# Performance work log

Measured on AMD Instinct MI355X. Metric: run time of the kernel, lower is better.

## Reference

```python
import jax, jax.numpy as jnp
import numpy as np

D_MODEL = 512
WINDOW = 8
N_LAYERS = 3
BATCH = 16384
EPS = 1e-12  # torch F.normalize eps


def _l2norm(x):
    # normalize over last axis, matching torch.nn.functional.normalize(p=2)
    n = jnp.sqrt(jnp.sum(x * x, axis=-1, keepdims=True))
    return x / jnp.maximum(n, EPS)


def setup_inputs() -> dict:
    key = jax.random.key(0)
    ks = jax.random.split(key, 14)
    d, w, L = D_MODEL, WINDOW, N_LAYERS
    s = 1.0 / np.sqrt(d)
    inp = {
        "x": jax.random.normal(ks[0], (BATCH, w + 1, d), dtype=jnp.float32),
        # stacked per-layer params
        "Wq": jax.random.normal(ks[1], (L, d, d), dtype=jnp.float32) * s,
        "bq": jax.random.normal(ks[2], (L, d), dtype=jnp.float32) * s,
        "Wk": jax.random.normal(ks[3], (L, w + 1, d, d), dtype=jnp.float32) * s,  # grouped conv: per-position linear
        "bk": jax.random.normal(ks[4], (L, w + 1, d), dtype=jnp.float32) * s,
        "Wfw": jax.random.normal(ks[5], (L, w, d, d), dtype=jnp.float32) * s,
        "bfw": jax.random.normal(ks[6], (L, w, d), dtype=jnp.float32) * s,
        "Wfc": jax.random.normal(ks[7], (L, d, d), dtype=jnp.float32) * s,
        "bfc": jax.random.normal(ks[8], (L, d), dtype=jnp.float32) * s,
        # final layer params
        "Wqf": jax.random.normal(ks[9], (d, d), dtype=jnp.float32) * s,
        "bqf": jax.random.normal(ks[10], (d,), dtype=jnp.float32) * s,
        "Wkf": jax.random.normal(ks[11], (w + 1, d, d), dtype=jnp.float32) * s,
        "bkf": jax.random.normal(ks[12], (w + 1, d), dtype=jnp.float32) * s,
    }
    return inp


def _attn_cent(x, Wq, bq, Wk, bk):
    # q: Linear on last position; k: grouped conv == per-position linear
    xc = x[:, -1, :]                                   # [B, d]
    q = xc @ Wq.T + bq                                 # [B, d]
    k = jnp.einsum('bpe,pde->bpd', x, Wk) + bk         # [B, W+1, d]
    attns = jax.nn.softmax(jnp.einsum('bd,bpd->bp', q, k), axis=-1)
    x_cent = jnp.einsum('bp,bpd->bd', attns, x)        # [B, d]
    return xc, x_cent


def _pt_layer(x, Wq, bq, Wk, bk, Wfw, bfw, Wfc, bfc):
    xc, x_cent = _attn_cent(x, Wq, bq, Wk, bk)
    x_cent = _l2norm(x_cent)
    x_cent = x_cent @ Wfc.T + bfc                      # ff_cent (dropout = identity, eval)
    x_cent = _l2norm(x_cent + xc)
    xw = x[:, :-1, :]                                  # [B, W, d]
    x_window = jnp.einsum('bpe,pde->bpd', xw, Wfw) + bfw + xw
    x_window = _l2norm(x_window)
    return jnp.concatenate([x_window, x_cent[:, None, :]], axis=1)


def reference(x, Wq, bq, Wk, bk, Wfw, bfw, Wfc, bfc, Wqf, bqf, Wkf, bkf):
    for l in range(N_LAYERS):
        x = _pt_layer(x, Wq[l], bq[l], Wk[l], bk[l], Wfw[l], bfw[l], Wfc[l], bfc[l])
    # final layer
    xc, x_cent = _attn_cent(x, Wqf, bqf, Wkf, bkf)
    return _l2norm((x_cent + xc)[:, None, :])          # [B, 1, d]
```

## Files before the change

### kernel.cpp

```cpp
#include <hip/hip_runtime.h>

#define BATCH_N 16384
#define PLANE 262144
typedef unsigned short ushort_t;
typedef __attribute__((ext_vector_type(4))) float f32x4;
typedef __attribute__((ext_vector_type(8))) short s16x8;
typedef __attribute__((ext_vector_type(4))) unsigned short u16x4;

__device__ inline void split_bf(float f, ushort_t& h, ushort_t& l) {
    unsigned u = __float_as_uint(f);
    h = (ushort_t)(u >> 16);
    float fh = __uint_as_float(u & 0xFFFF0000u);
    float r = f - fh;
    l = (ushort_t)(__float_as_uint(r) >> 16);
}

__global__ __launch_bounds__(256) void convert_w_k(
    const float* __restrict__ src, ushort_t* __restrict__ hi,
    ushort_t* __restrict__ lo, int n4)
{
    const int i = blockIdx.x * 256 + threadIdx.x;
    if (i >= n4) return;
    const f32x4 v = ((const f32x4*)src)[i];
    ushort_t h[4], l[4];
#pragma unroll
    for (int u = 0; u < 4; ++u) split_bf(v[u], h[u], l[u]);
    *(u16x4*)&hi[(size_t)i * 4] = (u16x4){h[0], h[1], h[2], h[3]};
    *(u16x4*)&lo[(size_t)i * 4] = (u16x4){l[0], l[1], l[2], l[3]};
}

template <int EPI>
__global__ __launch_bounds__(256, 3) void mfma_gemm_k(
    const float* __restrict__ A, int lda, int aoff,
    const ushort_t* __restrict__ Wh, const ushort_t* __restrict__ Wl,
    const float* __restrict__ bias, float* __restrict__ outp,
    const float* __restrict__ q, float* __restrict__ logits)
{
    __shared__ __align__(16) ushort_t Ah[128 * 40];
    __shared__ __align__(16) ushort_t Al[128 * 40];
    __shared__ __align__(16) ushort_t Bh[128 * 40];
    __shared__ __align__(16) ushort_t Bl[128 * 40];

    const int t = threadIdx.x;
    const int lane = t & 63, wave = t >> 6;
    const int wm = (wave >> 1) * 64, wn = (wave & 1) * 64;
    const int quad = lane >> 4, l15 = lane & 15;
    const size_t b0 = (size_t)blockIdx.x * 128;
    const int n0 = blockIdx.y * 128;
    int p = 0;
    if (EPI == 1) {
        p = blockIdx.z;
        Wh += (size_t)PLANE * p;
        Wl += (size_t)PLANE * p;
        aoff += p * 512;
    }

    f32x4 acc[4][4] = {};

    for (int k0 = 0; k0 < 512; k0 += 32) {
        f32x4 av[4];
        s16x8 bhv[2], blv[2];
#pragma unroll
        for (int u = 0; u < 4; ++u) {
            const int f = t + 256 * u, row = f >> 3, c = f & 7;
            av[u] = *(const f32x4*)&A[(b0 + row) * lda + aoff + k0 + c * 4];
        }
#pragma unroll
        for (int u = 0; u < 2; ++u) {
            const int f = t + 256 * u, row = f >> 2, c = f & 3;
            bhv[u] = *(const s16x8*)&Wh[(size_t)(n0 + row) * 512 + k0 + c * 8];
            blv[u] = *(const s16x8*)&Wl[(size_t)(n0 + row) * 512 + k0 + c * 8];
        }
        __syncthreads();
#pragma unroll
        for (int u = 0; u < 4; ++u) {
            const int f = t + 256 * u, row = f >> 3, c = f & 7;
            ushort_t h[4], l[4];
#pragma unroll
            for (int e = 0; e < 4; ++e) split_bf(av[u][e], h[e], l[e]);
            *(u16x4*)&Ah[row * 40 + c * 4] = (u16x4){h[0], h[1], h[2], h[3]};
            *(u16x4*)&Al[row * 40 + c * 4] = (u16x4){l[0], l[1], l[2], l[3]};
        }
#pragma unroll
        for (int u = 0; u < 2; ++u) {
            const int f = t + 256 * u, row = f >> 2, c = f & 3;
            *(s16x8*)&Bh[row * 40 + c * 8] = bhv[u];
            *(s16x8*)&Bl[row * 40 + c * 8] = blv[u];
        }
        __syncthreads();
        s16x8 ah[4], alo[4];
#pragma unroll
        for (int i = 0; i < 4; ++i) {
            ah[i]  = *(const s16x8*)&Ah[(wm + i * 16 + l15) * 40 + quad * 8];
            alo[i] = *(const s16x8*)&Al[(wm + i * 16 + l15) * 40 + quad * 8];
        }
#pragma unroll
        for (int j = 0; j < 4; ++j) {
            const s16x8 bh = *(const s16x8*)&Bh[(wn + j * 16 + l15) * 40 + quad * 8];
            const s16x8 bl = *(const s16x8*)&Bl[(wn + j * 16 + l15) * 40 + quad * 8];
#pragma unroll
            for (int i = 0; i < 4; ++i) {
                acc[i][j] = __builtin_amdgcn_mfma_f32_16x16x32_bf16(ah[i], bh, acc[i][j], 0, 0, 0);
                acc[i][j] = __builtin_amdgcn_mfma_f32_16x16x32_bf16(ah[i], bl, acc[i][j], 0, 0, 0);
                acc[i][j] = __builtin_amdgcn_mfma_f32_16x16x32_bf16(alo[i], bh, acc[i][j], 0, 0, 0);
            }
        }
    }

    if (EPI == 0) {
#pragma unroll
        for (int i = 0; i < 4; ++i) {
            const int gm0 = (int)b0 + wm + i * 16 + quad * 4;
#pragma unroll
            for (int j = 0; j < 4; ++j) {
                const int gn = n0 + wn + j * 16 + l15;
                const float bv = bias[gn];
#pragma unroll
                for (int r = 0; r < 4; ++r)
                    outp[(size_t)(gm0 + r) * 512 + gn] = acc[i][j][r] + bv;
            }
        }
    } else {
        float rp[4][4] = {};
#pragma unroll
        for (int i = 0; i < 4; ++i) {
            const int gm0 = (int)b0 + wm + i * 16 + quad * 4;
#pragma unroll
            for (int j = 0; j < 4; ++j) {
                const int gn = n0 + wn + j * 16 + l15;
                const float bv = bias[(size_t)p * 512 + gn];
#pragma unroll
                for (int r = 0; r < 4; ++r)
                    rp[i][r] += (acc[i][j][r] + bv) * q[(size_t)(gm0 + r) * 512 + gn];
            }
        }
#pragma unroll
        for (int m = 1; m < 16; m <<= 1)
#pragma unroll
            for (int i = 0; i < 4; ++i)
#pragma unroll
                for (int r = 0; r < 4; ++r)
                    rp[i][r] += __shfl_xor(rp[i][r], m, 64);
        if (l15 == 0) {
#pragma unroll
            for (int i = 0; i < 4; ++i) {
                const int gm0 = (int)b0 + wm + i * 16 + quad * 4;
#pragma unroll
                for (int r = 0; r < 4; ++r)
                    atomicAdd(&logits[(size_t)(gm0 + r) * 9 + p], rp[i][r]);
            }
        }
    }
}

__global__ __launch_bounds__(256) void softmax_cent_k(
    const float* __restrict__ x, const float* __restrict__ logits,
    float* __restrict__ outp, int mode)
{
    const int lane = threadIdx.x & 63;
    const size_t b = (size_t)blockIdx.x * 4 + (threadIdx.x >> 6);
    float lg[9], m = -1e30f;
#pragma unroll
    for (int p = 0; p < 9; ++p) { lg[p] = logits[b * 9 + p]; m = fmaxf(m, lg[p]); }
    float s = 0.f;
#pragma unroll
    for (int p = 0; p < 9; ++p) { lg[p] = __expf(lg[p] - m); s += lg[p]; }
    const float inv = 1.0f / s;
    f32x4 c[2];
    float ssq = 0.f;
#pragma unroll
    for (int v = 0; v < 2; ++v) {
        f32x4 a = {0.f, 0.f, 0.f, 0.f};
#pragma unroll
        for (int p = 0; p < 9; ++p) {
            const f32x4 xv = ((const f32x4*)&x[(b * 9 + p) * 512])[v * 64 + lane];
            a += lg[p] * xv;
        }
        a *= inv;
        if (mode) a += ((const f32x4*)&x[(b * 9 + 8) * 512])[v * 64 + lane];
        c[v] = a;
        ssq += a[0]*a[0] + a[1]*a[1] + a[2]*a[2] + a[3]*a[3];
    }
#pragma unroll
    for (int off = 32; off > 0; off >>= 1) ssq += __shfl_xor(ssq, off, 64);
    const float invn = 1.0f / fmaxf(sqrtf(ssq), 1e-12f);
#pragma unroll
    for (int v = 0; v < 2; ++v)
        ((f32x4*)&outp[b * 512])[v * 64 + lane] = c[v] * invn;
}

__global__ __launch_bounds__(256) void resid_norm_k(
    float* __restrict__ dst, int dstride, const float* __restrict__ src)
{
    const int lane = threadIdx.x & 63;
    const size_t b = (size_t)blockIdx.x * 4 + (threadIdx.x >> 6);
    f32x4* d4 = (f32x4*)&dst[b * (size_t)dstride];
    const f32x4* s4 = (const f32x4*)&src[b * 512];
    f32x4 a[2];
    float ssq = 0.f;
#pragma unroll
    for (int v = 0; v < 2; ++v) {
        a[v] = d4[v * 64 + lane] + s4[v * 64 + lane];
        ssq += a[v][0]*a[v][0] + a[v][1]*a[v][1] + a[v][2]*a[v][2] + a[v][3]*a[v][3];
    }
#pragma unroll
    for (int off = 32; off > 0; off >>= 1) ssq += __shfl_xor(ssq, off, 64);
    const float invn = 1.0f / fmaxf(sqrtf(ssq), 1e-12f);
#pragma unroll
    for (int v = 0; v < 2; ++v) d4[v * 64 + lane] = a[v] * invn;
}

extern "C" void kernel_launch(void* const* d_in, const int* in_sizes, int n_in,
                              void* d_out, int out_size, void* d_ws, size_t ws_size,
                              hipStream_t stream) {
    (void)in_sizes; (void)n_in; (void)out_size; (void)ws_size;
    float* x = (float*)d_in[0];
    const float* Wq  = (const float*)d_in[1];
    const float* bq  = (const float*)d_in[2];
    const float* Wk  = (const float*)d_in[3];
    const float* bk  = (const float*)d_in[4];
    const float* Wfw = (const float*)d_in[5];
    const float* bfw = (const float*)d_in[6];
    const float* Wfc = (const float*)d_in[7];
    const float* bfc = (const float*)d_in[8];
    const float* Wqf = (const float*)d_in[9];
    const float* bqf = (const float*)d_in[10];
    const float* Wkf = (const float*)d_in[11];
    const float* bkf = (const float*)d_in[12];
    float* out = (float*)d_out;

    ushort_t* whi = (ushort_t*)d_ws;
    ushort_t* wlo = whi + (size_t)67 * PLANE;
    float* fbuf   = (float*)(wlo + (size_t)67 * PLANE);
    float* q      = fbuf;
    float* cent   = q    + (size_t)BATCH_N * 512;
    float* y      = cent + (size_t)BATCH_N * 512;
    float* logits = y    + (size_t)BATCH_N * 512;
    float* tmp    = cent;

    const size_t OWq = 0, OWk = 3, OWfw = 30, OWfc = 54, OWqf = 57, OWkf = 58;

    struct { const float* s; size_t off; int cnt; } cv[6] = {
        {Wq, OWq, 3}, {Wk, OWk, 27}, {Wfw, OWfw, 24},
        {Wfc, OWfc, 3}, {Wqf, OWqf, 1}, {Wkf, OWkf, 9}};
    for (int i = 0; i < 6; ++i) {
        const int n4 = cv[i].cnt * PLANE / 4;
        convert_w_k<<<(n4 + 255) / 256, 256, 0, stream>>>(
            cv[i].s, whi + cv[i].off * PLANE, wlo + cv[i].off * PLANE, n4);
    }

    const dim3 gemm_grid(BATCH_N / 128, 4);
    const dim3 log_grid(BATCH_N / 128, 4, 9);
    const int ew_grid = BATCH_N / 4;

    for (int l = 0; l < 3; ++l) {
        mfma_gemm_k<0><<<gemm_grid, 256, 0, stream>>>(
            x, 9 * 512, 8 * 512,
            whi + (OWq + l) * PLANE, wlo + (OWq + l) * PLANE,
            bq + l * 512, q, nullptr, nullptr);
        hipMemsetAsync(logits, 0, (size_t)BATCH_N * 9 * sizeof(float), stream);
        mfma_gemm_k<1><<<log_grid, 256, 0, stream>>>(
            x, 9 * 512, 0,
            whi + (OWk + (size_t)l * 9) * PLANE, wlo + (OWk + (size_t)l * 9) * PLANE,
            bk + (size_t)l * 9 * 512, nullptr, q, logits);
        softmax_cent_k<<<ew_grid, 256, 0, stream>>>(x, logits, cent, 0);
        mfma_gemm_k<0><<<gemm_grid, 256, 0, stream>>>(
            cent, 512, 0,
            whi + (OWfc + l) * PLANE, wlo + (OWfc + l) * PLANE,
            bfc + l * 512, y, nullptr, nullptr);
        resid_norm_k<<<ew_grid, 256, 0, stream>>>(x + 8 * 512, 9 * 512, y);
        for (int p = 0; p < 8; ++p) {
            mfma_gemm_k<0><<<gemm_grid, 256, 0, stream>>>(
                x, 9 * 512, p * 512,
                whi + (OWfw + (size_t)l * 8 + p) * PLANE,
                wlo + (OWfw + (size_t)l * 8 + p) * PLANE,
                bfw + ((size_t)l * 8 + p) * 512, tmp, nullptr, nullptr);
            resid_norm_k<<<ew_grid, 256, 0, stream>>>(x + p * 512, 9 * 512, tmp);
        }
    }
    mfma_gemm_k<0><<<gemm_grid, 256, 0, stream>>>(
        x, 9 * 512, 8 * 512, whi + OWqf * PLANE, wlo + OWqf * PLANE,
        bqf, q, nullptr, nullptr);
    hipMemsetAsync(logits, 0, (size_t)BATCH_N * 9 * sizeof(float), stream);
    mfma_gemm_k<1><<<log_grid, 256, 0, stream>>>(
        x, 9 * 512, 0, whi + OWkf * PLANE, wlo + OWkf * PLANE,
        bkf, nullptr, q, logits);
    softmax_cent_k<<<ew_grid, 256, 0, stream>>>(x, logits, out, 1);
}
```

Before: 3.075 ms.

## Rewrite GEMM pipeline with fused residual-norm epilogues and packed split-bf16 activations

Replaces the 128x128 GEMM with a 64-row by full-512-column tile kernel that uses direct global-to-LDS loads for pre-swizzled weight planes. The residual add and L2 normalize are fused into the GEMM epilogue, which removes the separate resid_norm kernels and the temp buffers. The 8 per-position window GEMMs and the 9 key GEMMs now run as one grid each using the z dimension. Logits are reduced inside each block, so the atomics and the memset go away. Activations after layer 0 are stored in place as packed hi/lo bf16 words, which cuts conversion work but changes the in-memory format of x and relies on the in-place writes being race-free.

After: 3.336 ms. 8.5% more time.

```diff
diff --git a/kernel.cpp b/kernel.cpp
--- a/kernel.cpp
+++ b/kernel.cpp
@@ -1,213 +1,330 @@
 #include <hip/hip_runtime.h>
 
 #define BATCH_N 16384
+#define LDA 4608
 #define PLANE 262144
 typedef unsigned short ushort_t;
 typedef __attribute__((ext_vector_type(4))) float f32x4;
 typedef __attribute__((ext_vector_type(8))) short s16x8;
-typedef __attribute__((ext_vector_type(4))) unsigned short u16x4;
-
-__device__ inline void split_bf(float f, ushort_t& h, ushort_t& l) {
+typedef __attribute__((ext_vector_type(4))) unsigned u32x4;
+
+__device__ __forceinline__ void split_bf(float f, ushort_t& h, ushort_t& l) {
     unsigned u = __float_as_uint(f);
     h = (ushort_t)(u >> 16);
-    float fh = __uint_as_float(u & 0xFFFF0000u);
-    float r = f - fh;
+    float r = f - __uint_as_float(u & 0xFFFF0000u);
     l = (ushort_t)(__float_as_uint(r) >> 16);
+}
+__device__ __forceinline__ unsigned pack_bf(float f) {
+    unsigned u = __float_as_uint(f);
+    float r = f - __uint_as_float(u & 0xFFFF0000u);
+    return (u & 0xFFFF0000u) | (__float_as_uint(r) >> 16);
+}
+__device__ __forceinline__ float upack(unsigned u) {
+    return __uint_as_float(u & 0xFFFF0000u) + __uint_as_float(u << 16);
+}
+__device__ __forceinline__ s16x8 mk8(const ushort_t* v) {
+    return (s16x8){(short)v[0],(short)v[1],(short)v[2],(short)v[3],
+                   (short)v[4],(short)v[5],(short)v[6],(short)v[7]};
+}
+typedef __attribute__((address_space(3))) unsigned as3_u32;
+typedef __attribute__((address_space(1))) unsigned as1_u32;
+__device__ __forceinline__ void dma16(const ushort_t* g, ushort_t* l) {
+    __builtin_amdgcn_global_load_lds((as1_u32*)(unsigned long long)g,
+                                     (as3_u32*)(unsigned)(unsigned long long)l,
+                                     16, 0, 0);
 }
 
 __global__ __launch_bounds__(256) void convert_w_k(
     const float* __restrict__ src, ushort_t* __restrict__ hi,
-    ushort_t* __restrict__ lo, int n4)
+    ushort_t* __restrict__ lo, int total)
 {
-    const int i = blockIdx.x * 256 + threadIdx.x;
-    if (i >= n4) return;
-    const f32x4 v = ((const f32x4*)src)[i];
-    ushort_t h[4], l[4];
-#pragma unroll
-    for (int u = 0; u < 4; ++u) split_bf(v[u], h[u], l[u]);
-    *(u16x4*)&hi[(size_t)i * 4] = (u16x4){h[0], h[1], h[2], h[3]};
-    *(u16x4*)&lo[(size_t)i * 4] = (u16x4){l[0], l[1], l[2], l[3]};
-}
-
-template <int EPI>
-__global__ __launch_bounds__(256, 3) void mfma_gemm_k(
-    const float* __restrict__ A, int lda, int aoff,
-    const ushort_t* __restrict__ Wh, const ushort_t* __restrict__ Wl,
-    const float* __restrict__ bias, float* __restrict__ outp,
-    const float* __restrict__ q, float* __restrict__ logits)
+    const int gid = blockIdx.x * 256 + threadIdx.x;
+    if (gid >= total) return;
+    const int pp = gid >> 15;
+    const int rem = gid & 32767;
+    const int n = rem >> 6;
+    const int o = rem & 63;
+    const int chunk = o >> 2, oct = o & 3;
+    const float* s = src + (size_t)pp * PLANE + (size_t)n * 512 + o * 8;
+    const f32x4 f0 = *(const f32x4*)s;
+    const f32x4 f1 = *(const f32x4*)(s + 4);
+    ushort_t h[8], l[8];
+#pragma unroll
+    for (int e = 0; e < 4; ++e) {
+        split_bf(f0[e], h[e], l[e]);
+        split_bf(f1[e], h[4 + e], l[4 + e]);
+    }
+    const size_t d = (size_t)pp * PLANE + ((size_t)chunk * 512 + n) * 32
+                   + (size_t)((oct ^ (n & 3)) * 8);
+    *(s16x8*)&hi[d] = mk8(h);
+    *(s16x8*)&lo[d] = mk8(l);
+}
+
+template<int EPI, int AFMT, int RFMT>
+__global__ __launch_bounds__(256, 2) void gemm64_k(
+    const void* Ap, int lda, int aoff0, int a_zstep,
+    const ushort_t* __restrict__ Wh0, const ushort_t* __restrict__ Wl0,
+    const float* __restrict__ bias0,
+    float* __restrict__ outp,
+    const float* __restrict__ qv, float* __restrict__ logits,
+    void* resid, int rstride, int roff0)
 {
-    __shared__ __align__(16) ushort_t Ah[128 * 40];
-    __shared__ __align__(16) ushort_t Al[128 * 40];
-    __shared__ __align__(16) ushort_t Bh[128 * 40];
-    __shared__ __align__(16) ushort_t Bl[128 * 40];
+    __shared__ ushort_t smem[20480];
+    ushort_t* Bh = smem;
+    ushort_t* Bl = smem + 8192;
+    ushort_t* Ah = smem + 16384;
+    ushort_t* Al = smem + 18432;
 
     const int t = threadIdx.x;
-    const int lane = t & 63, wave = t >> 6;
-    const int wm = (wave >> 1) * 64, wn = (wave & 1) * 64;
+    const int lane = t & 63;
+    const int w = t >> 6;
     const int quad = lane >> 4, l15 = lane & 15;
-    const size_t b0 = (size_t)blockIdx.x * 128;
-    const int n0 = blockIdx.y * 128;
-    int p = 0;
-    if (EPI == 1) {
-        p = blockIdx.z;
-        Wh += (size_t)PLANE * p;
-        Wl += (size_t)PLANE * p;
-        aoff += p * 512;
-    }
-
-    f32x4 acc[4][4] = {};
-
-    for (int k0 = 0; k0 < 512; k0 += 32) {
-        f32x4 av[4];
-        s16x8 bhv[2], blv[2];
-#pragma unroll
-        for (int u = 0; u < 4; ++u) {
-            const int f = t + 256 * u, row = f >> 3, c = f & 7;
-            av[u] = *(const f32x4*)&A[(b0 + row) * lda + aoff + k0 + c * 4];
-        }
-#pragma unroll
-        for (int u = 0; u < 2; ++u) {
-            const int f = t + 256 * u, row = f >> 2, c = f & 3;
-            bhv[u] = *(const s16x8*)&Wh[(size_t)(n0 + row) * 512 + k0 + c * 8];
-            blv[u] = *(const s16x8*)&Wl[(size_t)(n0 + row) * 512 + k0 + c * 8];
+    const int b0 = blockIdx.x * 64;
+    const int pz = blockIdx.z;
+    const int aoff = aoff0 + pz * a_zstep;
+    const ushort_t* Wh = Wh0 + (size_t)pz * PLANE;
+    const ushort_t* Wl = Wl0 + (size_t)pz * PLANE;
+    const float* bias = bias0 + pz * 512;
+
+    const int arow = t >> 2;
+    const int aoct = t & 3;
+    const size_t abase = (size_t)(b0 + arow) * lda + aoff + aoct * 8;
+    const int adst = arow * 32 + ((aoct ^ (arow & 3)) * 8);
+
+    f32x4 acc[4][8] = {};
+
+    for (int c = 0; c < 16; ++c) {
+        ushort_t h8[8], l8[8];
+        if (AFMT == 1) {
+            const unsigned* Au = (const unsigned*)Ap;
+            const u32x4 u0 = *(const u32x4*)(Au + abase + (size_t)c * 32);
+            const u32x4 u1 = *(const u32x4*)(Au + abase + (size_t)c * 32 + 4);
+#pragma unroll
+            for (int e = 0; e < 4; ++e) {
+                h8[e] = (ushort_t)(u0[e] >> 16); l8[e] = (ushort_t)u0[e];
+                h8[4+e] = (ushort_t)(u1[e] >> 16); l8[4+e] = (ushort_t)u1[e];
+            }
+        } else {
+            const float* Af = (const float*)Ap;
+            const f32x4 f0 = *(const f32x4*)(Af + abase + (size_t)c * 32);
+            const f32x4 f1 = *(const f32x4*)(Af + abase + (size_t)c * 32 + 4);
+#pragma unroll
+            for (int e = 0; e < 4; ++e) {
+                split_bf(f0[e], h8[e], l8[e]);
+                split_bf(f1[e], h8[4+e], l8[4+e]);
+            }
+        }
+        s16x8 ah[4], av[4];
+#pragma unroll
+        for (int h = 0; h < 2; ++h) {
+            __syncthreads();
+            {
+                const size_t srow = ((size_t)c * 512 + h * 256 + w * 64) * 32
+                                  + (size_t)lane * 8;
+#pragma unroll
+                for (int u = 0; u < 4; ++u) {
+                    dma16(Wh + srow + u * 512, Bh + (w * 4 + u) * 512);
+                    dma16(Wl + srow + u * 512, Bl + (w * 4 + u) * 512);
+                }
+            }
+            if (h == 0) {
+                *(s16x8*)&Ah[adst] = mk8(h8);
+                *(s16x8*)&Al[adst] = mk8(l8);
+            }
+            __syncthreads();
+            if (h == 0) {
+#pragma unroll
+                for (int i = 0; i < 4; ++i) {
+                    const int rr = i * 16 + l15;
+                    const int ao = rr * 32 + ((quad ^ (rr & 3)) * 8);
+                    ah[i] = *(const s16x8*)&Ah[ao];
+                    av[i] = *(const s16x8*)&Al[ao];
+                }
+            }
+#pragma unroll
+            for (int j2 = 0; j2 < 4; ++j2) {
+                const int rn = w * 64 + j2 * 16 + l15;
+                const int bo = rn * 32 + ((quad ^ (rn & 3)) * 8);
+                const s16x8 bh = *(const s16x8*)&Bh[bo];
+                const s16x8 bl = *(const s16x8*)&Bl[bo];
+#pragma unroll
+                for (int i = 0; i < 4; ++i) {
+                    f32x4 a = acc[i][h * 4 + j2];
+                    a = __builtin_amdgcn_mfma_f32_16x16x32_bf16(av[i], bh, a, 0, 0, 0);
+                    a = __builtin_amdgcn_mfma_f32_16x16x32_bf16(ah[i], bl, a, 0, 0, 0);
+                    a = __builtin_amdgcn_mfma_f32_16x16x32_bf16(ah[i], bh, a, 0, 0, 0);
+                    acc[i][h * 4 + j2] = a;
+                }
+            }
+        }
+    }
+
+    __syncthreads();
+    float* red = (float*)smem;
+    float* nrm = (float*)smem + 256;
+
+    if (EPI == 0) {
+#pragma unroll
+        for (int i = 0; i < 4; ++i)
+#pragma unroll
+        for (int j = 0; j < 8; ++j) {
+            const int n = (j >> 2) * 256 + w * 64 + (j & 3) * 16 + l15;
+            const float bv = bias[n];
+#pragma unroll
+            for (int r = 0; r < 4; ++r) {
+                const int m = i * 16 + quad * 4 + r;
+                outp[(size_t)(b0 + m) * 512 + n] = acc[i][j][r] + bv;
+            }
+        }
+    } else if (EPI == 1) {
+        float rp[16];
+#pragma unroll
+        for (int v = 0; v < 16; ++v) rp[v] = 0.f;
+#pragma unroll
+        for (int j = 0; j < 8; ++j) {
+            const int n = (j >> 2) * 256 + w * 64 + (j & 3) * 16 + l15;
+            const float bv = bias[n];
+#pragma unroll
+            for (int i = 0; i < 4; ++i)
+#pragma unroll
+            for (int r = 0; r < 4; ++r) {
+                const int m = i * 16 + quad * 4 + r;
+                rp[i * 4 + r] += (acc[i][j][r] + bv) * qv[(size_t)(b0 + m) * 512 + n];
+            }
+        }
+#pragma unroll
+        for (int msk = 1; msk < 16; msk <<= 1)
+#pragma unroll
+            for (int v = 0; v < 16; ++v) rp[v] += __shfl_xor(rp[v], msk, 64);
+        if (l15 == 0) {
+#pragma unroll
+            for (int i = 0; i < 4; ++i)
+#pragma unroll
+            for (int r = 0; r < 4; ++r)
+                red[(i * 16 + quad * 4 + r) * 4 + w] = rp[i * 4 + r];
         }
         __syncthreads();
-#pragma unroll
-        for (int u = 0; u < 4; ++u) {
-            const int f = t + 256 * u, row = f >> 3, c = f & 7;
-            ushort_t h[4], l[4];
-#pragma unroll
-            for (int e = 0; e < 4; ++e) split_bf(av[u][e], h[e], l[e]);
-            *(u16x4*)&Ah[row * 40 + c * 4] = (u16x4){h[0], h[1], h[2], h[3]};
-            *(u16x4*)&Al[row * 40 + c * 4] = (u16x4){l[0], l[1], l[2], l[3]};
-        }
-#pragma unroll
-        for (int u = 0; u < 2; ++u) {
-            const int f = t + 256 * u, row = f >> 2, c = f & 3;
-            *(s16x8*)&Bh[row * 40 + c * 8] = bhv[u];
-            *(s16x8*)&Bl[row * 40 + c * 8] = blv[u];
+        if (t < 64)
+            logits[(size_t)(b0 + t) * 9 + pz] =
+                red[t * 4] + red[t * 4 + 1] + red[t * 4 + 2] + red[t * 4 + 3];
+    } else {
+        const int roffE = roff0 + pz * a_zstep;
+        float rp[16];
+#pragma unroll
+        for (int v = 0; v < 16; ++v) rp[v] = 0.f;
+#pragma unroll
+        for (int j = 0; j < 8; ++j) {
+            const int n = (j >> 2) * 256 + w * 64 + (j & 3) * 16 + l15;
+            const float bv = bias[n];
+#pragma unroll
+            for (int i = 0; i < 4; ++i)
+#pragma unroll
+            for (int r = 0; r < 4; ++r) {
+                const int m = i * 16 + quad * 4 + r;
+                const size_t ridx = (size_t)(b0 + m) * rstride + roffE + n;
+                const float rv = (RFMT == 1) ? upack(((const unsigned*)resid)[ridx])
+                                             : ((const float*)resid)[ridx];
+                const float v = acc[i][j][r] + bv + rv;
+                acc[i][j][r] = v;
+                rp[i * 4 + r] += v * v;
+            }
+        }
+#pragma unroll
+        for (int msk = 1; msk < 16; msk <<= 1)
+#pragma unroll
+            for (int v = 0; v < 16; ++v) rp[v] += __shfl_xor(rp[v], msk, 64);
+        if (l15 == 0) {
+#pragma unroll
+            for (int i = 0; i < 4; ++i)
+#pragma unroll
+            for (int r = 0; r < 4; ++r)
+                red[(i * 16 + quad * 4 + r) * 4 + w] = rp[i * 4 + r];
         }
         __syncthreads();
-        s16x8 ah[4], alo[4];
-#pragma unroll
-        for (int i = 0; i < 4; ++i) {
-            ah[i]  = *(const s16x8*)&Ah[(wm + i * 16 + l15) * 40 + quad * 8];
-            alo[i] = *(const s16x8*)&Al[(wm + i * 16 + l15) * 40 + quad * 8];
-        }
-#pragma unroll
-        for (int j = 0; j < 4; ++j) {
-            const s16x8 bh = *(const s16x8*)&Bh[(wn + j * 16 + l15) * 40 + quad * 8];
-            const s16x8 bl = *(const s16x8*)&Bl[(wn + j * 16 + l15) * 40 + quad * 8];
-#pragma unroll
-            for (int i = 0; i < 4; ++i) {
-                acc[i][j] = __builtin_amdgcn_mfma_f32_16x16x32_bf16(ah[i], bh, acc[i][j], 0, 0, 0);
-                acc[i][j] = __builtin_amdgcn_mfma_f32_16x16x32_bf16(ah[i], bl, acc[i][j], 0, 0, 0);
-                acc[i][j] = __builtin_amdgcn_mfma_f32_16x16x32_bf16(alo[i], bh, acc[i][j], 0, 0, 0);
-            }
-        }
-    }
-
-    if (EPI == 0) {
-#pragma unroll
-        for (int i = 0; i < 4; ++i) {
-            const int gm0 = (int)b0 + wm + i * 16 + quad * 4;
-#pragma unroll
-            for (int j = 0; j < 4; ++j) {
-                const int gn = n0 + wn + j * 16 + l15;
-                const float bv = bias[gn];
-#pragma unroll
-                for (int r = 0; r < 4; ++r)
-                    outp[(size_t)(gm0 + r) * 512 + gn] = acc[i][j][r] + bv;
-            }
-        }
-    } else {
-        float rp[4][4] = {};
-#pragma unroll
-        for (int i = 0; i < 4; ++i) {
-            const int gm0 = (int)b0 + wm + i * 16 + quad * 4;
-#pragma unroll
-            for (int j = 0; j < 4; ++j) {
-                const int gn = n0 + wn + j * 16 + l15;
-                const float bv = bias[(size_t)p * 512 + gn];
-#pragma unroll
-                for (int r = 0; r < 4; ++r)
-                    rp[i][r] += (acc[i][j][r] + bv) * q[(size_t)(gm0 + r) * 512 + gn];
-            }
-        }
-#pragma unroll
-        for (int m = 1; m < 16; m <<= 1)
-#pragma unroll
-            for (int i = 0; i < 4; ++i)
-#pragma unroll
-                for (int r = 0; r < 4; ++r)
-                    rp[i][r] += __shfl_xor(rp[i][r], m, 64);
-        if (l15 == 0) {
-#pragma unroll
-            for (int i = 0; i < 4; ++i) {
-                const int gm0 = (int)b0 + wm + i * 16 + quad * 4;
-#pragma unroll
-                for (int r = 0; r < 4; ++r)
-                    atomicAdd(&logits[(size_t)(gm0 + r) * 9 + p], rp[i][r]);
-            }
-        }
-    }
-}
-
+        if (t < 64) {
+            const float s = red[t * 4] + red[t * 4 + 1] + red[t * 4 + 2] + red[t * 4 + 3];
+            nrm[t] = 1.0f / fmaxf(sqrtf(s), 1e-12f);
+        }
+        __syncthreads();
+        unsigned* xw = (unsigned*)resid;
+#pragma unroll
+        for (int i = 0; i < 4; ++i)
+#pragma unroll
+        for (int r = 0; r < 4; ++r) {
+            const int m = i * 16 + quad * 4 + r;
+            const float s = nrm[m];
+#pragma unroll
+            for (int j = 0; j < 8; ++j) {
+                const int n = (j >> 2) * 256 + w * 64 + (j & 3) * 16 + l15;
+                xw[(size_t)(b0 + m) * rstride + roffE + n] = pack_bf(acc[i][j][r] * s);
+            }
+        }
+    }
+}
+
+template<int XFMT, int MODE>
 __global__ __launch_bounds__(256) void softmax_cent_k(
-    const float* __restrict__ x, const float* __restrict__ logits,
-    float* __restrict__ outp, int mode)
+    const void* xg, const float* __restrict__ logits, void* outp)
 {
     const int lane = threadIdx.x & 63;
     const size_t b = (size_t)blockIdx.x * 4 + (threadIdx.x >> 6);
-    float lg[9], m = -1e30f;
-#pragma unroll
-    for (int p = 0; p < 9; ++p) { lg[p] = logits[b * 9 + p]; m = fmaxf(m, lg[p]); }
+    float lg[9], mx = -1e30f;
+#pragma unroll
+    for (int p = 0; p < 9; ++p) { lg[p] = logits[b * 9 + p]; mx = fmaxf(mx, lg[p]); }
     float s = 0.f;
 #pragma unroll
-    for (int p = 0; p < 9; ++p) { lg[p] = __expf(lg[p] - m); s += lg[p]; }
+    for (int p = 0; p < 9; ++p) { lg[p] = __expf(lg[p] - mx); s += lg[p]; }
     const float inv = 1.0f / s;
-    f32x4 c[2];
+    float c[8];
     float ssq = 0.f;
 #pragma unroll
     for (int v = 0; v < 2; ++v) {
-        f32x4 a = {0.f, 0.f, 0.f, 0.f};
+        float a[4] = {0.f, 0.f, 0.f, 0.f};
+        float x8[4] = {0.f, 0.f, 0.f, 0.f};
 #pragma unroll
         for (int p = 0; p < 9; ++p) {
-            const f32x4 xv = ((const f32x4*)&x[(b * 9 + p) * 512])[v * 64 + lane];
-            a += lg[p] * xv;
-        }
-        a *= inv;
-        if (mode) a += ((const f32x4*)&x[(b * 9 + 8) * 512])[v * 64 + lane];
-        c[v] = a;
-        ssq += a[0]*a[0] + a[1]*a[1] + a[2]*a[2] + a[3]*a[3];
+            float f[4];
+            if (XFMT == 1) {
+                const u32x4 u = ((const u32x4*)xg)[(size_t)(b * 9 + p) * 128 + v * 64 + lane];
+#pragma unroll
+                for (int e = 0; e < 4; ++e) f[e] = upack(u[e]);
+            } else {
+                const f32x4 xv = ((const f32x4*)xg)[(size_t)(b * 9 + p) * 128 + v * 64 + lane];
+#pragma unroll
+                for (int e = 0; e < 4; ++e) f[e] = xv[e];
+            }
+#pragma unroll
+            for (int e = 0; e < 4; ++e) a[e] += lg[p] * f[e];
+            if (MODE == 1 && p == 8) {
+#pragma unroll
+                for (int e = 0; e < 4; ++e) x8[e] = f[e];
+            }
+        }
+#pragma unroll
+        for (int e = 0; e < 4; ++e) {
+            float av = a[e] * inv;
+            if (MODE == 1) av += x8[e];
+            c[v * 4 + e] = av;
+            ssq += av * av;
+        }
     }
 #pragma unroll
     for (int off = 32; off > 0; off >>= 1) ssq += __shfl_xor(ssq, off, 64);
     const float invn = 1.0f / fmaxf(sqrtf(ssq), 1e-12f);
 #pragma unroll
-    for (int v = 0; v < 2; ++v)
-        ((f32x4*)&outp[b * 512])[v * 64 + lane] = c[v] * invn;
-}
-
-__global__ __launch_bounds__(256) void resid_norm_k(
-    float* __restrict__ dst, int dstride, const float* __restrict__ src)
-{
-    const int lane = threadIdx.x & 63;
-    const size_t b = (size_t)blockIdx.x * 4 + (threadIdx.x >> 6);
-    f32x4* d4 = (f32x4*)&dst[b * (size_t)dstride];
-    const f32x4* s4 = (const f32x4*)&src[b * 512];
-    f32x4 a[2];
-    float ssq = 0.f;
-#pragma unroll
     for (int v = 0; v < 2; ++v) {
-        a[v] = d4[v * 64 + lane] + s4[v * 64 + lane];
-        ssq += a[v][0]*a[v][0] + a[v][1]*a[v][1] + a[v][2]*a[v][2] + a[v][3]*a[v][3];
-    }
-#pragma unroll
-    for (int off = 32; off > 0; off >>= 1) ssq += __shfl_xor(ssq, off, 64);
-    const float invn = 1.0f / fmaxf(sqrtf(ssq), 1e-12f);
-#pragma unroll
-    for (int v = 0; v < 2; ++v) d4[v * 64 + lane] = a[v] * invn;
+        if (MODE == 1) {
+            f32x4 o;
+#pragma unroll
+            for (int e = 0; e < 4; ++e) o[e] = c[v * 4 + e] * invn;
+            ((f32x4*)outp)[(size_t)b * 128 + v * 64 + lane] = o;
+        } else {
+            u32x4 o;
+#pragma unroll
+            for (int e = 0; e < 4; ++e) o[e] = pack_bf(c[v * 4 + e] * invn);
+            ((u32x4*)outp)[(size_t)b * 128 + v * 64 + lane] = o;
+        }
+    }
 }
 
 extern "C" void kernel_launch(void* const* d_in, const int* in_sizes, int n_in,
@@ -231,59 +348,56 @@
 
     ushort_t* whi = (ushort_t*)d_ws;
     ushort_t* wlo = whi + (size_t)67 * PLANE;
-    float* fbuf   = (float*)(wlo + (size_t)67 * PLANE);
-    float* q      = fbuf;
-    float* cent   = q    + (size_t)BATCH_N * 512;
-    float* y      = cent + (size_t)BATCH_N * 512;
-    float* logits = y    + (size_t)BATCH_N * 512;
-    float* tmp    = cent;
+    float* q       = (float*)(wlo + (size_t)67 * PLANE);
+    unsigned* cent = (unsigned*)(q + (size_t)BATCH_N * 512);
+    float* logits  = (float*)(cent + (size_t)BATCH_N * 512);
 
     const size_t OWq = 0, OWk = 3, OWfw = 30, OWfc = 54, OWqf = 57, OWkf = 58;
-
     struct { const float* s; size_t off; int cnt; } cv[6] = {
         {Wq, OWq, 3}, {Wk, OWk, 27}, {Wfw, OWfw, 24},
         {Wfc, OWfc, 3}, {Wqf, OWqf, 1}, {Wkf, OWkf, 9}};
-    for (int i = 0; i < 6; ++i) {
-        const int n4 = cv[i].cnt * PLANE / 4;
-        convert_w_k<<<(n4 + 255) / 256, 256, 0, stream>>>(
-            cv[i].s, whi + cv[i].off * PLANE, wlo + cv[i].off * PLANE, n4);
-    }
-
-    const dim3 gemm_grid(BATCH_N / 128, 4);
-    const dim3 log_grid(BATCH_N / 128, 4, 9);
-    const int ew_grid = BATCH_N / 4;
+    for (int i = 0; i < 6; ++i)
+        convert_w_k<<<cv[i].cnt * 128, 256, 0, stream>>>(
+            cv[i].s, whi + cv[i].off * PLANE, wlo + cv[i].off * PLANE,
+            cv[i].cnt * 32768);
+
+    const dim3 g1(BATCH_N / 64, 1, 1);
+    const dim3 g8(BATCH_N / 64, 1, 8);
+    const dim3 g9(BATCH_N / 64, 1, 9);
+    const int sg = BATCH_N / 4;
 
     for (int l = 0; l < 3; ++l) {
-        mfma_gemm_k<0><<<gemm_grid, 256, 0, stream>>>(
-            x, 9 * 512, 8 * 512,
-            whi + (OWq + l) * PLANE, wlo + (OWq + l) * PLANE,
-            bq + l * 512, q, nullptr, nullptr);
-        hipMemsetAsync(logits, 0, (size_t)BATCH_N * 9 * sizeof(float), stream);
-        mfma_gemm_k<1><<<log_grid, 256, 0, stream>>>(
-            x, 9 * 512, 0,
-            whi + (OWk + (size_t)l * 9) * PLANE, wlo + (OWk + (size_t)l * 9) * PLANE,
-            bk + (size_t)l * 9 * 512, nullptr, q, logits);
-        softmax_cent_k<<<ew_grid, 256, 0, stream>>>(x, logits, cent, 0);
-        mfma_gemm_k<0><<<gemm_grid, 256, 0, stream>>>(
-            cent, 512, 0,
-            whi + (OWfc + l) * PLANE, wlo + (OWfc + l) * PLANE,
-            bfc + l * 512, y, nullptr, nullptr);
-        resid_norm_k<<<ew_grid, 256, 0, stream>>>(x + 8 * 512, 9 * 512, y);
-        for (int p = 0; p < 8; ++p) {
-            mfma_gemm_k<0><<<gemm_grid, 256, 0, stream>>>(
-                x, 9 * 512, p * 512,
-                whi + (OWfw + (size_t)l * 8 + p) * PLANE,
-                wlo + (OWfw + (size_t)l * 8 + p) * PLANE,
-                bfw + ((size_t)l * 8 + p) * 512, tmp, nullptr, nullptr);
-            resid_norm_k<<<ew_grid, 256, 0, stream>>>(x + p * 512, 9 * 512, tmp);
-        }
-    }
-    mfma_gemm_k<0><<<gemm_grid, 256, 0, stream>>>(
-        x, 9 * 512, 8 * 512, whi + OWqf * PLANE, wlo + OWqf * PLANE,
-        bqf, q, nullptr, nullptr);
-    hipMemsetAsync(logits, 0, (size_t)BATCH_N * 9 * sizeof(float), stream);
-    mfma_gemm_k<1><<<log_grid, 256, 0, stream>>>(
-        x, 9 * 512, 0, whi + OWkf * PLANE, wlo + OWkf * PLANE,
-        bkf, nullptr, q, logits);
-    softmax_cent_k<<<ew_grid, 256, 0, stream>>>(x, logits, out, 1);
-}
+        const ushort_t* qh = whi + (OWq + l) * PLANE,  * ql = wlo + (OWq + l) * PLANE;
+        const ushort_t* kh = whi + (OWk + (size_t)l * 9) * PLANE,
+                      * kl = wlo + (OWk + (size_t)l * 9) * PLANE;
+        const ushort_t* ch = whi + (OWfc + l) * PLANE, * cl = wlo + (OWfc + l) * PLANE;
+        const ushort_t* fh = whi + (OWfw + (size_t)l * 8) * PLANE,
+                      * fl = wlo + (OWfw + (size_t)l * 8) * PLANE;
+        if (l == 0) {
+            gemm64_k<0,0,0><<<g1,256,0,stream>>>(x, LDA, 8*512, 0, qh, ql,
+                bq, q, nullptr, nullptr, nullptr, 0, 0);
+            gemm64_k<1,0,0><<<g9,256,0,stream>>>(x, LDA, 0, 512, kh, kl,
+                bk, nullptr, q, logits, nullptr, 0, 0);
+            softmax_cent_k<0,0><<<sg,256,0,stream>>>(x, logits, cent);
+            gemm64_k<2,1,0><<<g1,256,0,stream>>>(cent, 512, 0, 0, ch, cl,
+                bfc, nullptr, nullptr, nullptr, x, LDA, 8*512);
+            gemm64_k<2,0,0><<<g8,256,0,stream>>>(x, LDA, 0, 512, fh, fl,
+                bfw, nullptr, nullptr, nullptr, x, LDA, 0);
+        } else {
+            gemm64_k<0,1,0><<<g1,256,0,stream>>>(x, LDA, 8*512, 0, qh, ql,
+                bq + l*512, q, nullptr, nullptr, nullptr, 0, 0);
+            gemm64_k<1,1,0><<<g9,256,0,stream>>>(x, LDA, 0, 512, kh, kl,
+                bk + (size_t)l*9*512, nullptr, q, logits, nullptr, 0, 0);
+            softmax_cent_k<1,0><<<sg,256,0,stream>>>(x, logits, cent);
+            gemm64_k<2,1,1><<<g1,256,0,stream>>>(cent, 512, 0, 0, ch, cl,
+                bfc + l*512, nullptr, nullptr, nullptr, x, LDA, 8*512);
+            gemm64_k<2,1,1><<<g8,256,0,stream>>>(x, LDA, 0, 512, fh, fl,
+                bfw + (size_t)l*8*512, nullptr, nullptr, nullptr, x, LDA, 0);
+        }
+    }
+    gemm64_k<0,1,0><<<g1,256,0,stream>>>(x, LDA, 8*512, 0,
+        whi + OWqf*PLANE, wlo + OWqf*PLANE, bqf, q, nullptr, nullptr, nullptr, 0, 0);
+    gemm64_k<1,1,0><<<g9,256,0,stream>>>(x, LDA, 0, 512,
+        whi + OWkf*PLANE, wlo + OWkf*PLANE, bkf, nullptr, q, logits, nullptr, 0, 0);
+    softmax_cent_k<1,1><<<sg,256,0,stream>>>(x, logits, out);
+}
```
